# Performance work log

Hardware: AMD Instinct MI355X
Metric: run time of the kernel (lower is better)

## Reference

```python
import jax, jax.numpy as jnp
import numpy as np

B, G, K, C, NT = 128, 64, 32, 256, 8192


def setup_inputs() -> dict:
    key = jax.random.key(0)
    ks = jax.random.split(key, 8)
    s = lambda fan_in: 1.0 / np.sqrt(fan_in)
    return {
        "patch_features": jax.random.normal(ks[0], (B, G, C), jnp.float32),
        "neighborhood": jax.random.normal(ks[1], (B, G, K, 3), jnp.float32),
        "codebook": jax.random.normal(ks[2], (NT, C), jnp.float32),
        "w1": jax.random.normal(ks[3], (512, C), jnp.float32) * s(C),
        "b1": jnp.zeros((512,), jnp.float32),
        "w2": jax.random.normal(ks[4], (256, 512), jnp.float32) * s(512),
        "b2": jnp.zeros((256,), jnp.float32),
        "w3": jax.random.normal(ks[5], (3 * K, 256), jnp.float32) * s(256),
        "b3": jnp.zeros((3 * K,), jnp.float32),
    }


def reference(patch_features, neighborhood, codebook, w1, b1, w2, b2, w3, b3):
    b, g, c = patch_features.shape
    k = neighborhood.shape[2]
    # squared euclidean distances to codebook (argmin equals argmin of cdist p=2)
    d2 = (
        jnp.sum(patch_features * patch_features, -1, keepdims=True)
        - 2.0 * jnp.einsum("bgc,nc->bgn", patch_features, codebook)
        + jnp.sum(codebook * codebook, -1)
    )  # [B,G,NT]
    token_ids = jnp.argmin(d2, axis=-1)          # [B,G]
    quantized = codebook[token_ids]              # [B,G,C] gather
    # 1x1 Conv1d stack == per-token MLP
    h = jax.nn.relu(jnp.einsum("bgc,oc->bgo", quantized, w1) + b1)
    h = jax.nn.relu(jnp.einsum("bgc,oc->bgo", h, w2) + b2)
    rec = jnp.einsum("bgc,oc->bgo", h, w3) + b3  # [B,G,3K]
    rec = rec.reshape(b * g, k, 3)
    gt = neighborhood.reshape(b * g, k, 3)
    # Chamfer distance L2 (squared) both directions
    diff = rec[:, :, None, :] - gt[:, None, :, :]  # [BG,K,K,3]
    dd = jnp.sum(diff * diff, -1)                  # [BG,K,K]
    loss = jnp.mean(jnp.min(dd, axis=2)) + jnp.mean(jnp.min(dd, axis=1))
    return loss
```

## Files before the change

kernel.cpp:

```cpp
#include <hip/hip_runtime.h>
#include <hip/hip_bf16.h>
#include <float.h>

#define NTOK 8192
#define NCB  8192
#define CDIM 256
#define KPTS 32
#define SQNT 24.0f
#define INV_CFOLD (SQNT * SQNT * 64.0f)

typedef __attribute__((ext_vector_type(8))) short short8;
typedef __attribute__((ext_vector_type(4))) float f32x4;
typedef __attribute__((ext_vector_type(4))) int i32x4;
typedef unsigned int u32;
typedef unsigned long long u64;

__device__ __forceinline__ void gl_lds16(const void* g, void* l) {
  __builtin_amdgcn_global_load_lds(
      (const __attribute__((address_space(1))) u32*)(g),
      (__attribute__((address_space(3))) u32*)(l), 16, 0, 0);
}

__device__ __forceinline__ ushort bf16_rne(float x) {
  u32 u = __float_as_uint(x);
  return (ushort)((u + 0x7fffu + ((u >> 16) & 1u)) >> 16);
}

__device__ __forceinline__ int pack4i8(int a, int b, int c, int d) {
  return (a & 0xff) | ((b & 0xff) << 8) | ((c & 0xff) << 16) | ((d & 0xff) << 24);
}

__global__ __launch_bounds__(256) void prep_k(
    const float* __restrict__ pf, const float* __restrict__ cb,
    const float* __restrict__ w1, const float* __restrict__ w2,
    const float* __restrict__ w3,
    i32x4* __restrict__ pf1, i32x4* __restrict__ pf2,
    i32x4* __restrict__ cb1, i32x4* __restrict__ cb2,
    ushort* __restrict__ cb_bf, ushort* __restrict__ w1s,
    ushort* __restrict__ w2s, ushort* __restrict__ w3s,
    float* __restrict__ cnorm) {
  int gid = blockIdx.x * 4 + (threadIdx.x >> 6);
  int lane = threadIdx.x & 63, r16 = lane & 15, quad = lane >> 4;
  if (gid < 4096) {
    bool is_cb = gid >= 2048;
    int t = is_cb ? gid - 2048 : gid;
    int tile = t >> 2, kb = t & 3;
    const float* src = is_cb ? cb : pf;
    int row = tile * 16 + r16;
    const float* sp = src + (size_t)row * CDIM + kb * 64 + quad * 16;
    float4 v0 = ((const float4*)sp)[0];
    float4 v1 = ((const float4*)sp)[1];
    float4 v2 = ((const float4*)sp)[2];
    float4 v3 = ((const float4*)sp)[3];
    float x[16] = {v0.x, v0.y, v0.z, v0.w, v1.x, v1.y, v1.z, v1.w,
                   v2.x, v2.y, v2.z, v2.w, v3.x, v3.y, v3.z, v3.w};
    int q1[16], q2[16];
    float s = 0.f;
#pragma unroll
    for (int e = 0; e < 16; e++) {
      float as = x[e] * SQNT;
      float a1 = rintf(as);
      a1 = fminf(fmaxf(a1, -127.f), 127.f);
      float a2 = rintf((as - a1) * 128.f);
      a2 = fminf(fmaxf(a2, -127.f), 127.f);
      q1[e] = (int)a1;
      q2[e] = (int)a2;
      s += x[e] * x[e];
    }
    i32x4 p1 = {pack4i8(q1[0], q1[1], q1[2], q1[3]),
                pack4i8(q1[4], q1[5], q1[6], q1[7]),
                pack4i8(q1[8], q1[9], q1[10], q1[11]),
                pack4i8(q1[12], q1[13], q1[14], q1[15])};
    i32x4 p2 = {pack4i8(q2[0], q2[1], q2[2], q2[3]),
                pack4i8(q2[4], q2[5], q2[6], q2[7]),
                pack4i8(q2[8], q2[9], q2[10], q2[11]),
                pack4i8(q2[12], q2[13], q2[14], q2[15])};
    size_t o = (size_t)t * 64 + lane;
    (is_cb ? cb1 : pf1)[o] = p1;
    (is_cb ? cb2 : pf2)[o] = p2;
    if (is_cb) {
      s += __shfl_xor(s, 16, 64);
      s += __shfl_xor(s, 32, 64);
      if (quad == 0) atomicAdd(cnorm + row, s);
    }
  } else if (gid < 8192) {
    int t = gid - 4096;
    int tile = t >> 3, kb = t & 7;
    int row = tile * 16 + r16;
    const float* sp = cb + (size_t)row * CDIM + kb * 32 + quad * 8;
    float4 a = ((const float4*)sp)[0];
    float4 b = ((const float4*)sp)[1];
    short8 vh = {(short)bf16_rne(a.x), (short)bf16_rne(a.y),
                 (short)bf16_rne(a.z), (short)bf16_rne(a.w),
                 (short)bf16_rne(b.x), (short)bf16_rne(b.y),
                 (short)bf16_rne(b.z), (short)bf16_rne(b.w)};
    *(short8*)(cb_bf + ((size_t)tile * 8 + kb) * 512 + lane * 8) = vh;
  } else if (gid < 8752) {
    int t = gid - 8192;
    const float* src;
    ushort* dst;
    int KB;
    if (t < 256)      { src = w1; dst = w1s; KB = 8; }
    else if (t < 512) { src = w2; dst = w2s; KB = 16; t -= 256; }
    else              { src = w3; dst = w3s; KB = 8;  t -= 512; }
    int tile = t / KB, kb = t - tile * KB, K = KB * 32;
    int row = tile * 16 + r16;
    const float* sp = src + (size_t)row * K + kb * 32 + quad * 8;
    float4 a = ((const float4*)sp)[0];
    float4 b = ((const float4*)sp)[1];
    short8 vh = {(short)bf16_rne(a.x), (short)bf16_rne(a.y),
                 (short)bf16_rne(a.z), (short)bf16_rne(a.w),
                 (short)bf16_rne(b.x), (short)bf16_rne(b.y),
                 (short)bf16_rne(b.z), (short)bf16_rne(b.w)};
    *(short8*)(dst + ((size_t)tile * KB + kb) * 512 + lane * 8) = vh;
  }
}

__global__ __launch_bounds__(256, 2) void argmin_k(
    const char* __restrict__ A1g, const char* __restrict__ A2g,
    const char* __restrict__ B1g, const char* __restrict__ B2g,
    const float* __restrict__ cnorm, u64* __restrict__ pkeys) {
  __shared__ char lds[32 * 1024];
  int tid = threadIdx.x;
  int ns = blockIdx.x, mt = blockIdx.y;
  int wv = tid >> 6, lane = tid & 63;
  int quad = lane >> 4, r16 = lane & 15;
  int wr = wv >> 1, wc = wv & 1;

  int bvi[4][4], bii[4][4];
#pragma unroll
  for (int i = 0; i < 4; i++)
#pragma unroll
    for (int r = 0; r < 4; r++) { bvi[i][r] = 0x7fffffff; bii[i][r] = 0x7fffffff; }

  const char* bsrc = (wv == 0) ? A1g : (wv == 1) ? A2g : (wv == 2) ? B1g : B2g;

  for (int nts = 0; nts < 4; ++nts) {
    int nt = ns * 4 + nts;
    i32x4 am[4][4], ac[4][4];
#pragma unroll
    for (int i = 0; i < 4; i++)
#pragma unroll
      for (int j = 0; j < 4; j++) {
        am[i][j] = (i32x4){0, 0, 0, 0};
        ac[i][j] = (i32x4){0, 0, 0, 0};
      }
    for (int kb = 0; kb < 4; ++kb) {
#pragma unroll
      for (int u = 0; u < 8; ++u) {
        int gt = ((wv < 2) ? mt : nt) * 8 + u;
        gl_lds16(bsrc + ((size_t)gt * 4 + kb) * 1024 + lane * 16,
                 lds + (wv * 8 + u) * 1024);
      }
      __syncthreads();
      i32x4 f1[4], f2[4], g1[4], g2[4];
#pragma unroll
      for (int i = 0; i < 4; i++) {
        f1[i] = *(const i32x4*)(lds + (wr * 4 + i) * 1024 + lane * 16);
        f2[i] = *(const i32x4*)(lds + (8 + wr * 4 + i) * 1024 + lane * 16);
      }
#pragma unroll
      for (int j = 0; j < 4; j++) {
        g1[j] = *(const i32x4*)(lds + (16 + wc * 4 + j) * 1024 + lane * 16);
        g2[j] = *(const i32x4*)(lds + (24 + wc * 4 + j) * 1024 + lane * 16);
      }
#pragma unroll
      for (int i = 0; i < 4; i++)
#pragma unroll
        for (int j = 0; j < 4; j++) {
          am[i][j] = __builtin_amdgcn_mfma_i32_16x16x64_i8(f1[i], g1[j], am[i][j], 0, 0, 0);
          ac[i][j] = __builtin_amdgcn_mfma_i32_16x16x64_i8(f1[i], g2[j], ac[i][j], 0, 0, 0);
          ac[i][j] = __builtin_amdgcn_mfma_i32_16x16x64_i8(f2[i], g1[j], ac[i][j], 0, 0, 0);
        }
      __syncthreads();
    }
#pragma unroll
    for (int j = 0; j < 4; j++) {
      int col = nt * 128 + wc * 64 + j * 16 + r16;
      int cni = __float2int_rn(cnorm[col] * INV_CFOLD);
#pragma unroll
      for (int i = 0; i < 4; i++)
#pragma unroll
        for (int r = 0; r < 4; r++) {
          int di = cni - (am[i][j][r] * 128 + ac[i][j][r]);
          if (di < bvi[i][r]) { bvi[i][r] = di; bii[i][r] = col; }
        }
    }
  }
#pragma unroll
  for (int m = 1; m < 16; m <<= 1) {
#pragma unroll
    for (int i = 0; i < 4; i++)
#pragma unroll
      for (int r = 0; r < 4; r++) {
        int ov = __shfl_xor(bvi[i][r], m, 64);
        int oi = __shfl_xor(bii[i][r], m, 64);
        if (ov < bvi[i][r] || (ov == bvi[i][r] && oi < bii[i][r])) {
          bvi[i][r] = ov;
          bii[i][r] = oi;
        }
      }
  }
  if (r16 == 0) {
#pragma unroll
    for (int i = 0; i < 4; i++)
#pragma unroll
      for (int r = 0; r < 4; r++) {
        int row = mt * 128 + wr * 64 + i * 16 + quad * 4 + r;
        u32 mk = (u32)(bvi[i][r] + (1 << 30));
        pkeys[(size_t)(ns * 2 + wc) * NTOK + row] = ((u64)mk << 32) | (u32)bii[i][r];
      }
  }
}

__global__ __launch_bounds__(256) void mlp_fused_k(
    const u64* __restrict__ pkeys, const ushort* __restrict__ cb_bf,
    const ushort* __restrict__ w1s, const float* __restrict__ b1,
    const ushort* __restrict__ w2s, const float* __restrict__ b2,
    const ushort* __restrict__ w3s, const float* __restrict__ b3,
    const float* __restrict__ neigh, float* __restrict__ out) {
  __shared__ char lds[65536];
  __shared__ int ids[32];
  __shared__ float wsum[4];
  ushort* qsp = (ushort*)lds;
  ushort* h1p = (ushort*)(lds + 16384);
  ushort* h2p = (ushort*)(lds + 49152);
  float* recp = (float*)lds;
  float* gtsp = (float*)(lds + 16384);

  int tid = threadIdx.x;
  int t0 = blockIdx.x * 32;
  int wv = tid >> 6, lane = tid & 63;
  int quad = lane >> 4, r16 = lane & 15;
  int mtile = wv >> 1, nh = wv & 1;

  {
    int row_l = tid >> 3, sl = tid & 7;
    u64 best = ~0ull;
#pragma unroll
    for (int s = 0; s < 4; s++) {
      u64 v = pkeys[(size_t)(sl + s * 8) * NTOK + t0 + row_l];
      if (v < best) best = v;
    }
#pragma unroll
    for (int m = 1; m < 8; m <<= 1) {
      u64 o = __shfl_xor((unsigned long long)best, m, 64);
      if (o < best) best = o;
    }
    if (sl == 0) ids[row_l] = (int)(u32)best;
  }
  __syncthreads();

  {
    int tile_l = wv >> 1, kb0 = (wv & 1) * 4;
    int id = ids[tile_l * 16 + r16];
#pragma unroll
    for (int q = 0; q < 4; q++) {
      int kb = kb0 + q;
      short8 v = *(const short8*)(cb_bf + ((size_t)(id >> 4) * 8 + kb) * 512 +
                                  (size_t)((id & 15) + quad * 16) * 8);
      *(short8*)(qsp + (size_t)(tile_l * 8 + kb) * 512 + lane * 8) = v;
    }
  }
  __syncthreads();

  {
    short8 fa[8];
#pragma unroll
    for (int kb = 0; kb < 8; kb++)
      fa[kb] = *(const short8*)(qsp + (size_t)(mtile * 8 + kb) * 512 + lane * 8);
    for (int jt = nh * 16; jt < nh * 16 + 16; ++jt) {
      f32x4 acc = (f32x4){0.f, 0.f, 0.f, 0.f};
#pragma unroll
      for (int kb = 0; kb < 8; kb++) {
        short8 fb = *(const short8*)(w1s + ((size_t)jt * 8 + kb) * 512 + lane * 8);
        acc = __builtin_amdgcn_mfma_f32_16x16x32_bf16(fa[kb], fb, acc, 0, 0, 0);
      }
      int col = jt * 16 + r16;
      float bj = b1[col];
#pragma unroll
      for (int reg = 0; reg < 4; reg++) {
        int row_l = mtile * 16 + quad * 4 + reg;
        float v = fmaxf(acc[reg] + bj, 0.f);
        size_t o = (size_t)((row_l >> 4) * 16 + (col >> 5)) * 512 +
                   (size_t)(((col >> 3) & 3) * 16 + (row_l & 15)) * 8 + (col & 7);
        h1p[o] = bf16_rne(v);
      }
    }
  }
  __syncthreads();

  {
    short8 fa[16];
#pragma unroll
    for (int kb = 0; kb < 16; kb++)
      fa[kb] = *(const short8*)(h1p + (size_t)(mtile * 16 + kb) * 512 + lane * 8);
    for (int jt = nh * 8; jt < nh * 8 + 8; ++jt) {
      f32x4 acc = (f32x4){0.f, 0.f, 0.f, 0.f};
#pragma unroll
      for (int kb = 0; kb < 16; kb++) {
        short8 fb = *(const short8*)(w2s + ((size_t)jt * 16 + kb) * 512 + lane * 8);
        acc = __builtin_amdgcn_mfma_f32_16x16x32_bf16(fa[kb], fb, acc, 0, 0, 0);
      }
      int col = jt * 16 + r16;
      float bj = b2[col];
#pragma unroll
      for (int reg = 0; reg < 4; reg++) {
        int row_l = mtile * 16 + quad * 4 + reg;
        float v = fmaxf(acc[reg] + bj, 0.f);
        size_t o = (size_t)((row_l >> 4) * 8 + (col >> 5)) * 512 +
                   (size_t)(((col >> 3) & 3) * 16 + (row_l & 15)) * 8 + (col & 7);
        h2p[o] = bf16_rne(v);
      }
    }
  }
  __syncthreads();

#pragma unroll
  for (int s = 0; s < 3; s++) {
    int idx = tid + s * 256;
    int t = idx / 24, c = (idx - t * 24) * 4;
    *(float4*)(gtsp + (size_t)t * 96 + c) =
        *(const float4*)(neigh + (size_t)(t0 + t) * 96 + c);
  }

  {
    short8 fa[8];
#pragma unroll
    for (int kb = 0; kb < 8; kb++)
      fa[kb] = *(const short8*)(h2p + (size_t)(mtile * 8 + kb) * 512 + lane * 8);
#pragma unroll
    for (int jj = 0; jj < 3; ++jj) {
      int jt = nh * 3 + jj;
      f32x4 acc = (f32x4){0.f, 0.f, 0.f, 0.f};
#pragma unroll
      for (int kb = 0; kb < 8; kb++) {
        short8 fb = *(const short8*)(w3s + ((size_t)jt * 8 + kb) * 512 + lane * 8);
        acc = __builtin_amdgcn_mfma_f32_16x16x32_bf16(fa[kb], fb, acc, 0, 0, 0);
      }
      int col = jt * 16 + r16;
      float bj = b3[col];
#pragma unroll
      for (int reg = 0; reg < 4; reg++) {
        int row_l = mtile * 16 + quad * 4 + reg;
        recp[(size_t)row_l * 96 + col] = acc[reg] + bj;
      }
    }
  }
  __syncthreads();

  float local = 0.f;
#pragma unroll
  for (int pp = 0; pp < 4; ++pp) {
    int p = tid + pp * 256;
    int t = p >> 5, i = p & 31;
    float rx = recp[t * 96 + 3 * i], ry = recp[t * 96 + 3 * i + 1], rz = recp[t * 96 + 3 * i + 2];
    float gx = gtsp[t * 96 + 3 * i], gy = gtsp[t * 96 + 3 * i + 1], gz = gtsp[t * 96 + 3 * i + 2];
    float mA = FLT_MAX, mB = FLT_MAX;
#pragma unroll
    for (int j = 0; j < 32; j++) {
      float dx = rx - gtsp[t * 96 + 3 * j], dy = ry - gtsp[t * 96 + 3 * j + 1],
            dz = rz - gtsp[t * 96 + 3 * j + 2];
      float d = dx * dx + dy * dy + dz * dz;
      mA = fminf(mA, d);
      dx = recp[t * 96 + 3 * j] - gx; dy = recp[t * 96 + 3 * j + 1] - gy;
      dz = recp[t * 96 + 3 * j + 2] - gz;
      d = dx * dx + dy * dy + dz * dz;
      mB = fminf(mB, d);
    }
    local += mA + mB;
  }
#pragma unroll
  for (int off = 32; off; off >>= 1) local += __shfl_down(local, off, 64);
  if ((tid & 63) == 0) wsum[tid >> 6] = local;
  __syncthreads();
  if (tid == 0) {
    float s = wsum[0] + wsum[1] + wsum[2] + wsum[3];
    atomicAdd(out, s * (1.0f / (float)(NTOK * KPTS)));
  }
}

extern "C" void kernel_launch(void* const* d_in, const int* in_sizes, int n_in,
                              void* d_out, int out_size, void* d_ws, size_t ws_size,
                              hipStream_t stream) {
  const float* pf    = (const float*)d_in[0];
  const float* neigh = (const float*)d_in[1];
  const float* cb    = (const float*)d_in[2];
  const float* w1    = (const float*)d_in[3];
  const float* b1    = (const float*)d_in[4];
  const float* w2    = (const float*)d_in[5];
  const float* b2    = (const float*)d_in[6];
  const float* w3    = (const float*)d_in[7];
  const float* b3    = (const float*)d_in[8];
  float* out = (float*)d_out;
  char* base = (char*)d_ws;

  u64*   pkeys = (u64*)base;
  float* cnorm = (float*)(base + 0x200000);
  char*  pf1   = base + 0x210000;
  char*  pf2   = base + 0x410000;
  char*  cb1   = base + 0x610000;
  char*  cb2   = base + 0x810000;
  ushort* cb_bf = (ushort*)(base + 0xA10000);
  ushort* w1s   = (ushort*)(base + 0xE10000);
  ushort* w2s   = (ushort*)(base + 0xE50000);
  ushort* w3s   = (ushort*)(base + 0xE90000);

  hipMemsetAsync(d_out, 0, sizeof(float), stream);
  hipMemsetAsync(cnorm, 0, NCB * sizeof(float), stream);
  prep_k<<<2188, 256, 0, stream>>>(pf, cb, w1, w2, w3,
                                   (i32x4*)pf1, (i32x4*)pf2, (i32x4*)cb1,
                                   (i32x4*)cb2, cb_bf, w1s, w2s, w3s, cnorm);
  argmin_k<<<dim3(16, 64), 256, 0, stream>>>(pf1, pf2, cb1, cb2, cnorm, pkeys);
  mlp_fused_k<<<256, 256, 0, stream>>>(pkeys, cb_bf, w1s, b1, w2s, b2, w3s, b3,
                                       neigh, out);
}
```

Baseline: 170.0 us.

## Split fused MLP into gather and tiled GEMM kernels; fold bf16 codebook into prep

Replaces the single fused per-32-token MLP kernel, launched as only 256 blocks, with separate gather, GEMM1, GEMM2 and GEMM3+chamfer kernels. The GEMMs are tiled across a 2D grid with LDS staging via global_load_lds and double-buffered A tiles, aiming for more parallelism and more weight reuse. The prep kernel now writes the bf16 codebook while quantizing and reduces codebook norms in LDS rather than with atomics, which removes the memset and the extra codebook pass. In exchange, h1 and h2 now round-trip through global memory, and the extra kernel launches add overhead.

```diff
diff --git a/kernel.cpp b/kernel.cpp
--- a/kernel.cpp
+++ b/kernel.cpp
@@ -39,7 +39,9 @@
     ushort* __restrict__ cb_bf, ushort* __restrict__ w1s,
     ushort* __restrict__ w2s, ushort* __restrict__ w3s,
     float* __restrict__ cnorm) {
+  __shared__ float cred[4][16];
   int gid = blockIdx.x * 4 + (threadIdx.x >> 6);
+  int wv = threadIdx.x >> 6;
   int lane = threadIdx.x & 63, r16 = lane & 15, quad = lane >> 4;
   if (gid < 4096) {
     bool is_cb = gid >= 2048;
@@ -79,24 +81,33 @@
     (is_cb ? cb1 : pf1)[o] = p1;
     (is_cb ? cb2 : pf2)[o] = p2;
     if (is_cb) {
+      int kb32 = 2 * kb + (quad >> 1);
+      int slot0 = ((2 * quad) & 3) * 16 + r16;
+      int slot1 = ((2 * quad + 1) & 3) * 16 + r16;
+      size_t bo = ((size_t)tile * 8 + kb32) * 512;
+      short8 vh0 = {(short)bf16_rne(x[0]), (short)bf16_rne(x[1]),
+                    (short)bf16_rne(x[2]), (short)bf16_rne(x[3]),
+                    (short)bf16_rne(x[4]), (short)bf16_rne(x[5]),
+                    (short)bf16_rne(x[6]), (short)bf16_rne(x[7])};
+      short8 vh1 = {(short)bf16_rne(x[8]), (short)bf16_rne(x[9]),
+                    (short)bf16_rne(x[10]), (short)bf16_rne(x[11]),
+                    (short)bf16_rne(x[12]), (short)bf16_rne(x[13]),
+                    (short)bf16_rne(x[14]), (short)bf16_rne(x[15])};
+      *(short8*)(cb_bf + bo + (size_t)slot0 * 8) = vh0;
+      *(short8*)(cb_bf + bo + (size_t)slot1 * 8) = vh1;
       s += __shfl_xor(s, 16, 64);
       s += __shfl_xor(s, 32, 64);
-      if (quad == 0) atomicAdd(cnorm + row, s);
-    }
-  } else if (gid < 8192) {
+      if (quad == 0) cred[wv][r16] = s;
+      __syncthreads();
+      if (threadIdx.x < 16) {
+        int ctile = blockIdx.x - 512;
+        cnorm[ctile * 16 + threadIdx.x] =
+            cred[0][threadIdx.x] + cred[1][threadIdx.x] +
+            cred[2][threadIdx.x] + cred[3][threadIdx.x];
+      }
+    }
+  } else if (gid < 4656) {
     int t = gid - 4096;
-    int tile = t >> 3, kb = t & 7;
-    int row = tile * 16 + r16;
-    const float* sp = cb + (size_t)row * CDIM + kb * 32 + quad * 8;
-    float4 a = ((const float4*)sp)[0];
-    float4 b = ((const float4*)sp)[1];
-    short8 vh = {(short)bf16_rne(a.x), (short)bf16_rne(a.y),
-                 (short)bf16_rne(a.z), (short)bf16_rne(a.w),
-                 (short)bf16_rne(b.x), (short)bf16_rne(b.y),
-                 (short)bf16_rne(b.z), (short)bf16_rne(b.w)};
-    *(short8*)(cb_bf + ((size_t)tile * 8 + kb) * 512 + lane * 8) = vh;
-  } else if (gid < 8752) {
-    int t = gid - 8192;
     const float* src;
     ushort* dst;
     int KB;
@@ -213,138 +224,223 @@
   }
 }
 
-__global__ __launch_bounds__(256) void mlp_fused_k(
-    const u64* __restrict__ pkeys, const ushort* __restrict__ cb_bf,
-    const ushort* __restrict__ w1s, const float* __restrict__ b1,
-    const ushort* __restrict__ w2s, const float* __restrict__ b2,
-    const ushort* __restrict__ w3s, const float* __restrict__ b3,
-    const float* __restrict__ neigh, float* __restrict__ out) {
-  __shared__ char lds[65536];
-  __shared__ int ids[32];
-  __shared__ float wsum[4];
-  ushort* qsp = (ushort*)lds;
-  ushort* h1p = (ushort*)(lds + 16384);
-  ushort* h2p = (ushort*)(lds + 49152);
-  float* recp = (float*)lds;
-  float* gtsp = (float*)(lds + 16384);
-
+__global__ __launch_bounds__(256) void gather_k(const u64* __restrict__ pkeys,
+                                                const ushort* __restrict__ cb_bf,
+                                                ushort* __restrict__ quant) {
+  int gid = blockIdx.x * 4 + (threadIdx.x >> 6);
+  int lane = threadIdx.x & 63, r16 = lane & 15, quad = lane >> 4;
+  int tile = gid >> 3, kb = gid & 7;
+  int row = tile * 16 + r16;
+  u64 best = pkeys[row];
+#pragma unroll
+  for (int s = 1; s < 32; s++) {
+    u64 v = pkeys[(size_t)s * NTOK + row];
+    if (v < best) best = v;
+  }
+  int id = (int)(u32)best;
+  short8 v = *(const short8*)(cb_bf + ((size_t)(id >> 4) * 8 + kb) * 512 +
+                              (size_t)((id & 15) + quad * 16) * 8);
+  *(short8*)(quant + ((size_t)tile * 8 + kb) * 512 + lane * 8) = v;
+}
+
+__global__ __launch_bounds__(256, 3) void gemm1_k(
+    const ushort* __restrict__ quant, const ushort* __restrict__ w1s,
+    const float* __restrict__ b1, ushort* __restrict__ h1) {
+  __shared__ ushort Bs[32 * 512];
+  __shared__ ushort As[2][8 * 512];
   int tid = threadIdx.x;
-  int t0 = blockIdx.x * 32;
+  int nt = blockIdx.x, mt = blockIdx.y;
   int wv = tid >> 6, lane = tid & 63;
   int quad = lane >> 4, r16 = lane & 15;
-  int mtile = wv >> 1, nh = wv & 1;
-
-  {
-    int row_l = tid >> 3, sl = tid & 7;
-    u64 best = ~0ull;
-#pragma unroll
-    for (int s = 0; s < 4; s++) {
-      u64 v = pkeys[(size_t)(sl + s * 8) * NTOK + t0 + row_l];
-      if (v < best) best = v;
-    }
-#pragma unroll
-    for (int m = 1; m < 8; m <<= 1) {
-      u64 o = __shfl_xor((unsigned long long)best, m, 64);
-      if (o < best) best = o;
-    }
-    if (sl == 0) ids[row_l] = (int)(u32)best;
+
+#pragma unroll
+  for (int u = 0; u < 8; ++u) {
+    int c = wv + u * 4;
+    int jt = nt * 4 + (c >> 3), kb = c & 7;
+    gl_lds16(w1s + ((size_t)jt * 8 + kb) * 512 + lane * 8, Bs + (size_t)c * 512);
+  }
+#pragma unroll
+  for (int v = 0; v < 2; ++v) {
+    int c = wv * 2 + v;
+    gl_lds16(quant + ((size_t)(mt * 8 + c) * 8 + 0) * 512 + lane * 8,
+             As[0] + (size_t)c * 512);
   }
   __syncthreads();
 
-  {
-    int tile_l = wv >> 1, kb0 = (wv & 1) * 4;
-    int id = ids[tile_l * 16 + r16];
-#pragma unroll
-    for (int q = 0; q < 4; q++) {
-      int kb = kb0 + q;
-      short8 v = *(const short8*)(cb_bf + ((size_t)(id >> 4) * 8 + kb) * 512 +
-                                  (size_t)((id & 15) + quad * 16) * 8);
-      *(short8*)(qsp + (size_t)(tile_l * 8 + kb) * 512 + lane * 8) = v;
-    }
+  f32x4 acc[2][4];
+#pragma unroll
+  for (int i = 0; i < 2; i++)
+#pragma unroll
+    for (int j = 0; j < 4; j++) acc[i][j] = (f32x4){0.f, 0.f, 0.f, 0.f};
+
+  for (int kb = 0; kb < 8; ++kb) {
+    if (kb < 7) {
+#pragma unroll
+      for (int v = 0; v < 2; ++v) {
+        int c = wv * 2 + v;
+        gl_lds16(quant + ((size_t)(mt * 8 + c) * 8 + kb + 1) * 512 + lane * 8,
+                 As[(kb + 1) & 1] + (size_t)c * 512);
+      }
+    }
+    const ushort* A = As[kb & 1];
+    short8 fa[2], fb[4];
+#pragma unroll
+    for (int i = 0; i < 2; i++)
+      fa[i] = *(const short8*)(A + (size_t)(wv * 2 + i) * 512 + lane * 8);
+#pragma unroll
+    for (int j = 0; j < 4; j++)
+      fb[j] = *(const short8*)(Bs + (size_t)(j * 8 + kb) * 512 + lane * 8);
+#pragma unroll
+    for (int i = 0; i < 2; i++)
+#pragma unroll
+      for (int j = 0; j < 4; j++)
+        acc[i][j] = __builtin_amdgcn_mfma_f32_16x16x32_bf16(fa[i], fb[j], acc[i][j], 0, 0, 0);
+    __syncthreads();
+  }
+
+#pragma unroll
+  for (int j = 0; j < 4; j++) {
+    int col = nt * 64 + j * 16 + r16;
+    float bj = b1[col];
+#pragma unroll
+    for (int i = 0; i < 2; i++) {
+#pragma unroll
+      for (int reg = 0; reg < 4; reg++) {
+        int row = mt * 128 + (wv * 2 + i) * 16 + quad * 4 + reg;
+        float v = fmaxf(acc[i][j][reg] + bj, 0.f);
+        size_t o = ((size_t)(row >> 4) * 16 + (col >> 5)) * 512 +
+                   (size_t)(((col >> 3) & 3) * 16 + (row & 15)) * 8 + (col & 7);
+        h1[o] = bf16_rne(v);
+      }
+    }
+  }
+}
+
+__global__ __launch_bounds__(256, 3) void gemm2_k(
+    const ushort* __restrict__ h1, const ushort* __restrict__ w2s,
+    const float* __restrict__ b2, ushort* __restrict__ h2) {
+  __shared__ ushort Bs[32 * 512];
+  __shared__ ushort As[2][8 * 512];
+  int tid = threadIdx.x;
+  int nt = blockIdx.x, mt = blockIdx.y;
+  int wv = tid >> 6, lane = tid & 63;
+  int quad = lane >> 4, r16 = lane & 15;
+
+#pragma unroll
+  for (int u = 0; u < 8; ++u) {
+    int c = wv + u * 4;
+    int jt = nt * 2 + (c >> 4), kb = c & 15;
+    gl_lds16(w2s + ((size_t)jt * 16 + kb) * 512 + lane * 8, Bs + (size_t)c * 512);
+  }
+#pragma unroll
+  for (int v = 0; v < 2; ++v) {
+    int c = wv * 2 + v;
+    gl_lds16(h1 + ((size_t)(mt * 8 + c) * 16 + 0) * 512 + lane * 8,
+             As[0] + (size_t)c * 512);
   }
   __syncthreads();
 
-  {
-    short8 fa[8];
-#pragma unroll
-    for (int kb = 0; kb < 8; kb++)
-      fa[kb] = *(const short8*)(qsp + (size_t)(mtile * 8 + kb) * 512 + lane * 8);
-    for (int jt = nh * 16; jt < nh * 16 + 16; ++jt) {
-      f32x4 acc = (f32x4){0.f, 0.f, 0.f, 0.f};
-#pragma unroll
-      for (int kb = 0; kb < 8; kb++) {
-        short8 fb = *(const short8*)(w1s + ((size_t)jt * 8 + kb) * 512 + lane * 8);
-        acc = __builtin_amdgcn_mfma_f32_16x16x32_bf16(fa[kb], fb, acc, 0, 0, 0);
-      }
-      int col = jt * 16 + r16;
-      float bj = b1[col];
+  f32x4 acc[2][2];
+#pragma unroll
+  for (int i = 0; i < 2; i++)
+#pragma unroll
+    for (int j = 0; j < 2; j++) acc[i][j] = (f32x4){0.f, 0.f, 0.f, 0.f};
+
+  for (int kb = 0; kb < 16; ++kb) {
+    if (kb < 15) {
+#pragma unroll
+      for (int v = 0; v < 2; ++v) {
+        int c = wv * 2 + v;
+        gl_lds16(h1 + ((size_t)(mt * 8 + c) * 16 + kb + 1) * 512 + lane * 8,
+                 As[(kb + 1) & 1] + (size_t)c * 512);
+      }
+    }
+    const ushort* A = As[kb & 1];
+    short8 fa[2], fb[2];
+#pragma unroll
+    for (int i = 0; i < 2; i++)
+      fa[i] = *(const short8*)(A + (size_t)(wv * 2 + i) * 512 + lane * 8);
+#pragma unroll
+    for (int j = 0; j < 2; j++)
+      fb[j] = *(const short8*)(Bs + (size_t)(j * 16 + kb) * 512 + lane * 8);
+#pragma unroll
+    for (int i = 0; i < 2; i++)
+#pragma unroll
+      for (int j = 0; j < 2; j++)
+        acc[i][j] = __builtin_amdgcn_mfma_f32_16x16x32_bf16(fa[i], fb[j], acc[i][j], 0, 0, 0);
+    __syncthreads();
+  }
+
+#pragma unroll
+  for (int j = 0; j < 2; j++) {
+    int col = nt * 32 + j * 16 + r16;
+    float bj = b2[col];
+#pragma unroll
+    for (int i = 0; i < 2; i++) {
 #pragma unroll
       for (int reg = 0; reg < 4; reg++) {
-        int row_l = mtile * 16 + quad * 4 + reg;
-        float v = fmaxf(acc[reg] + bj, 0.f);
-        size_t o = (size_t)((row_l >> 4) * 16 + (col >> 5)) * 512 +
-                   (size_t)(((col >> 3) & 3) * 16 + (row_l & 15)) * 8 + (col & 7);
-        h1p[o] = bf16_rne(v);
-      }
-    }
-  }
-  __syncthreads();
-
-  {
-    short8 fa[16];
-#pragma unroll
-    for (int kb = 0; kb < 16; kb++)
-      fa[kb] = *(const short8*)(h1p + (size_t)(mtile * 16 + kb) * 512 + lane * 8);
-    for (int jt = nh * 8; jt < nh * 8 + 8; ++jt) {
-      f32x4 acc = (f32x4){0.f, 0.f, 0.f, 0.f};
-#pragma unroll
-      for (int kb = 0; kb < 16; kb++) {
-        short8 fb = *(const short8*)(w2s + ((size_t)jt * 16 + kb) * 512 + lane * 8);
-        acc = __builtin_amdgcn_mfma_f32_16x16x32_bf16(fa[kb], fb, acc, 0, 0, 0);
-      }
-      int col = jt * 16 + r16;
-      float bj = b2[col];
-#pragma unroll
-      for (int reg = 0; reg < 4; reg++) {
-        int row_l = mtile * 16 + quad * 4 + reg;
-        float v = fmaxf(acc[reg] + bj, 0.f);
-        size_t o = (size_t)((row_l >> 4) * 8 + (col >> 5)) * 512 +
-                   (size_t)(((col >> 3) & 3) * 16 + (row_l & 15)) * 8 + (col & 7);
-        h2p[o] = bf16_rne(v);
-      }
-    }
-  }
-  __syncthreads();
-
+        int row = mt * 128 + (wv * 2 + i) * 16 + quad * 4 + reg;
+        float v = fmaxf(acc[i][j][reg] + bj, 0.f);
+        size_t o = ((size_t)(row >> 4) * 8 + (col >> 5)) * 512 +
+                   (size_t)(((col >> 3) & 3) * 16 + (row & 15)) * 8 + (col & 7);
+        h2[o] = bf16_rne(v);
+      }
+    }
+  }
+}
+
+__global__ __launch_bounds__(256) void gemm3_chamfer_k(
+    const ushort* __restrict__ h2, const ushort* __restrict__ w3s,
+    const float* __restrict__ b3, const float* __restrict__ neigh,
+    float* __restrict__ out) {
+  extern __shared__ char lds[];
+  ushort* Bs = (ushort*)lds;
+  ushort* As = (ushort*)(lds + 49152);
+  float* recp = (float*)(lds + 65536);
+  float* gtsp = (float*)(lds + 77824);
+  float* wsum = (float*)(lds + 90112);
+  int tid = threadIdx.x;
+  int mt = blockIdx.x;
+  int wv = tid >> 6, lane = tid & 63;
+  int quad = lane >> 4, r16 = lane & 15;
+
+#pragma unroll
+  for (int u = 0; u < 12; ++u) {
+    int c = wv + u * 4;
+    gl_lds16(w3s + (size_t)c * 512 + lane * 8, Bs + (size_t)c * 512);
+  }
+#pragma unroll
+  for (int v = 0; v < 4; ++v) {
+    int c = wv * 4 + v;
+    gl_lds16(h2 + ((size_t)(mt * 2 + (c >> 3)) * 8 + (c & 7)) * 512 + lane * 8,
+             As + (size_t)c * 512);
+  }
 #pragma unroll
   for (int s = 0; s < 3; s++) {
     int idx = tid + s * 256;
     int t = idx / 24, c = (idx - t * 24) * 4;
     *(float4*)(gtsp + (size_t)t * 96 + c) =
-        *(const float4*)(neigh + (size_t)(t0 + t) * 96 + c);
-  }
-
-  {
-    short8 fa[8];
-#pragma unroll
-    for (int kb = 0; kb < 8; kb++)
-      fa[kb] = *(const short8*)(h2p + (size_t)(mtile * 8 + kb) * 512 + lane * 8);
-#pragma unroll
-    for (int jj = 0; jj < 3; ++jj) {
-      int jt = nh * 3 + jj;
-      f32x4 acc = (f32x4){0.f, 0.f, 0.f, 0.f};
-#pragma unroll
-      for (int kb = 0; kb < 8; kb++) {
-        short8 fb = *(const short8*)(w3s + ((size_t)jt * 8 + kb) * 512 + lane * 8);
-        acc = __builtin_amdgcn_mfma_f32_16x16x32_bf16(fa[kb], fb, acc, 0, 0, 0);
-      }
-      int col = jt * 16 + r16;
-      float bj = b3[col];
-#pragma unroll
-      for (int reg = 0; reg < 4; reg++) {
-        int row_l = mtile * 16 + quad * 4 + reg;
-        recp[(size_t)row_l * 96 + col] = acc[reg] + bj;
-      }
+        *(const float4*)(neigh + (size_t)(mt * 32 + t) * 96 + c);
+  }
+  __syncthreads();
+
+#pragma unroll
+  for (int w = 0; w < 3; ++w) {
+    int p = wv + w * 4;
+    int i = p / 6, j = p - i * 6;
+    f32x4 acc = (f32x4){0.f, 0.f, 0.f, 0.f};
+#pragma unroll
+    for (int kb = 0; kb < 8; kb++) {
+      short8 fa = *(const short8*)(As + (size_t)(i * 8 + kb) * 512 + lane * 8);
+      short8 fb = *(const short8*)(Bs + (size_t)(j * 8 + kb) * 512 + lane * 8);
+      acc = __builtin_amdgcn_mfma_f32_16x16x32_bf16(fa, fb, acc, 0, 0, 0);
+    }
+    int col = j * 16 + r16;
+    float bj = b3[col];
+#pragma unroll
+    for (int reg = 0; reg < 4; reg++) {
+      int row_l = i * 16 + quad * 4 + reg;
+      recp[(size_t)row_l * 96 + col] = acc[reg] + bj;
     }
   }
   __syncthreads();
@@ -372,7 +468,7 @@
   }
 #pragma unroll
   for (int off = 32; off; off >>= 1) local += __shfl_down(local, off, 64);
-  if ((tid & 63) == 0) wsum[tid >> 6] = local;
+  if (lane == 0) wsum[wv] = local;
   __syncthreads();
   if (tid == 0) {
     float s = wsum[0] + wsum[1] + wsum[2] + wsum[3];
@@ -405,13 +501,17 @@
   ushort* w1s   = (ushort*)(base + 0xE10000);
   ushort* w2s   = (ushort*)(base + 0xE50000);
   ushort* w3s   = (ushort*)(base + 0xE90000);
+  ushort* quant = (ushort*)(base + 0x210000);
+  ushort* h1    = (ushort*)(base + 0x610000);
+  ushort* h2    = (ushort*)(base + 0xF00000);
 
   hipMemsetAsync(d_out, 0, sizeof(float), stream);
-  hipMemsetAsync(cnorm, 0, NCB * sizeof(float), stream);
-  prep_k<<<2188, 256, 0, stream>>>(pf, cb, w1, w2, w3,
+  prep_k<<<1164, 256, 0, stream>>>(pf, cb, w1, w2, w3,
                                    (i32x4*)pf1, (i32x4*)pf2, (i32x4*)cb1,
                                    (i32x4*)cb2, cb_bf, w1s, w2s, w3s, cnorm);
   argmin_k<<<dim3(16, 64), 256, 0, stream>>>(pf1, pf2, cb1, cb2, cnorm, pkeys);
-  mlp_fused_k<<<256, 256, 0, stream>>>(pkeys, cb_bf, w1s, b1, w2s, b2, w3s, b3,
-                                       neigh, out);
-}
+  gather_k<<<1024, 256, 0, stream>>>(pkeys, cb_bf, quant);
+  gemm1_k<<<dim3(8, 64), 256, 0, stream>>>(quant, w1s, b1, h1);
+  gemm2_k<<<dim3(8, 64), 256, 0, stream>>>(h1, w2s, b2, h2);
+  gemm3_chamfer_k<<<256, 256, 90128, stream>>>(h2, w3s, b3, neigh, out);
+}
```

After: 188.9 us. 1.11x slower.
